# Kernel optimization log

Hardware: AMD Instinct MI355X
Metric: run time of the kernel (lower is better)

The kernel has to match this reference:

```python
import jax, jax.numpy as jnp
import numpy as np

B, T, I, H = 64, 256, 512, 800
RATE = 0.5


def setup_inputs() -> dict:
    key = jax.random.key(0)
    ks = jax.random.split(key, 9)
    x = jax.random.normal(ks[0], (B, T, I), dtype=jnp.float32)
    # Keras LSTM dropout: 4 per-gate Bernoulli masks on the input, constant over time
    mask_f = jax.random.bernoulli(ks[1], 1.0 - RATE, (B, 4, I)).astype(jnp.float32) / (1.0 - RATE)
    mask_b = jax.random.bernoulli(ks[2], 1.0 - RATE, (B, 4, I)).astype(jnp.float32) / (1.0 - RATE)
    s_w = 1.0 / np.sqrt(I)
    s_u = 1.0 / np.sqrt(H)
    W_f = jax.random.normal(ks[3], (I, 4 * H), dtype=jnp.float32) * s_w
    U_f = jax.random.normal(ks[4], (H, 4 * H), dtype=jnp.float32) * s_u
    W_b = jax.random.normal(ks[5], (I, 4 * H), dtype=jnp.float32) * s_w
    U_b = jax.random.normal(ks[6], (H, 4 * H), dtype=jnp.float32) * s_u
    # Keras unit_forget_bias: forget-gate bias = 1 (gate order i, f, c, o)
    b = jnp.concatenate([jnp.zeros(H), jnp.ones(H), jnp.zeros(H), jnp.zeros(H)]).astype(jnp.float32)
    return {"x": x, "mask_f": mask_f, "mask_b": mask_b,
            "W_f": W_f, "U_f": U_f, "b_f": b, "W_b": W_b, "U_b": U_b, "b_b": b}


def _lstm(x, W, U, b, mask):
    """x:(B,T,I) W:(I,4H) U:(H,4H) b:(4H,) mask:(B,4,I) -> (B,T,H), h, c."""
    b_, t_, i_ = x.shape
    h_ = U.shape[0]
    # per-gate input dropout, projections precomputed for all timesteps
    xd = x[:, :, None, :] * mask[:, None, :, :]                 # (B,T,4,I)
    proj = jnp.einsum('btgi,igh->btgh', xd, W.reshape(i_, 4, h_))
    proj = proj + b.reshape(4, h_)                              # (B,T,4,H)

    def step(carry, p):
        h, c = carry
        z = p + (h @ U).reshape(b_, 4, h_)                      # (B,4,H)
        i = jax.nn.sigmoid(z[:, 0])
        f = jax.nn.sigmoid(z[:, 1])
        g = jnp.tanh(z[:, 2])
        o = jax.nn.sigmoid(z[:, 3])
        c = f * c + i * g
        h = o * jnp.tanh(c)
        return (h, c), h

    h0 = jnp.zeros((b_, h_), x.dtype)
    c0 = jnp.zeros((b_, h_), x.dtype)
    (h, c), Hs = jax.lax.scan(step, (h0, c0), jnp.swapaxes(proj, 0, 1))
    return jnp.swapaxes(Hs, 0, 1), h, c


def reference(x, mask_f, mask_b, W_f, U_f, b_f, W_b, U_b, b_b):
    H1, h1, c1 = _lstm(x, W_f, U_f, b_f, mask_f)
    # go_backwards=True: process reversed sequence; Keras returns outputs in
    # processing (reversed) order and the model concatenates directly.
    H2, h2, c2 = _lstm(x[:, ::-1], W_b, U_b, b_b, mask_b)
    Hcat = jnp.concatenate([H1, H2], axis=2)
    hcat = jnp.concatenate([h1, h2], axis=1)
    ccat = jnp.concatenate([c1, c2], axis=1)
    return (Hcat, hcat, ccat)
```

## Files before the change

### kernel.cpp

```cpp
#include <hip/hip_runtime.h>


#define TDIM 256
#define IDIM 512
#define HDIM 800
#define H4   3200

typedef __bf16 bf16;
typedef __bf16 bf16x8 __attribute__((ext_vector_type(8)));
typedef __bf16 bf16x4 __attribute__((ext_vector_type(4)));
typedef float  f32x4  __attribute__((ext_vector_type(4)));
typedef unsigned int u32x4 __attribute__((ext_vector_type(4)));
typedef unsigned int u32x2 __attribute__((ext_vector_type(2)));

#define OFF_UPK   0ull
#define OFF_WPK   10240000ull
#define OFF_PROJB 16793600ull
#define OFF_HA    121651200ull
#define OFF_FLAGS 174284800ull
#define WS_NEED   174297600ull

__device__ __forceinline__ float sigf(float x)   { return 1.0f / (1.0f + __expf(-x)); }
__device__ __forceinline__ float tanhf_f(float x){ return 2.0f / (1.0f + __expf(-2.0f*x)) - 1.0f; }

__device__ __forceinline__ void store_b128_sc1(void* p, u32x4 v) {
    asm volatile("global_store_dwordx4 %0, %1, off sc1" :: "v"(p), "v"(v) : "memory");
}

__global__ __launch_bounds__(256) void kinit(uint4* __restrict__ ha0,
                                             uint4* __restrict__ flg) {
    int idx = blockIdx.x * 256 + threadIdx.x;
    if (idx < 12800) ha0[idx] = uint4{0u, 0u, 0u, 0u};
    else if (idx < 13600) flg[idx - 12800] = uint4{0u, 0u, 0u, 0u};
}

__global__ __launch_bounds__(64) void kpack(const float* __restrict__ Sf,
                                            const float* __restrict__ Sb,
                                            bf16* __restrict__ dst, int nkt) {
    int bx = blockIdx.x;
    int kt = bx % nkt; int rest = bx / nkt;
    int nt = rest % 200; int d = rest / 200;
    const float* S = d ? Sb : Sf;
    int l  = threadIdx.x;
    int n  = nt * 16 + (l & 15);
    int k0 = kt * 32 + (l >> 4) * 8;
    bf16x8 v;
#pragma unroll
    for (int j = 0; j < 8; ++j) v[j] = (bf16)S[(size_t)(k0 + j) * H4 + n];
    *(bf16x8*)(dst + ((size_t)bx * 64 + l) * 8) = v;
}

#define K1ROW 520
__global__ __launch_bounds__(256, 1) void kproj(
    const float* __restrict__ x, const float* __restrict__ mf, const float* __restrict__ mb,
    const bf16* __restrict__ wpk, const float* __restrict__ biasf, const float* __restrict__ biasb,
    bf16* __restrict__ projf, bf16* __restrict__ projb) {
    __shared__ bf16 sA[64 * K1ROW];

    int bx = blockIdx.x;
    int jj = bx % 5; int tt = (bx / 5) & 3; int g = (bx / 20) & 3;
    int b  = (bx / 80) & 63; int d = bx / 5120;

    int t  = threadIdx.x;
    int wv = t >> 6, l = t & 63;

    const float* mask = (d ? mb : mf) + (size_t)(b * 4 + g) * IDIM;
    int k = l * 8;
    float4 m0 = *(const float4*)(mask + k);
    float4 m1 = *(const float4*)(mask + k + 4);

    for (int it = 0; it < 16; ++it) {
        int trow = it * 4 + wv;
        int tg   = tt * 64 + trow;
        int te   = d ? (255 - tg) : tg;
        const float* xs = x + ((size_t)b * TDIM + te) * IDIM + k;
        float4 x0 = *(const float4*)xs;
        float4 x1 = *(const float4*)(xs + 4);
        bf16x8 v;
        v[0] = (bf16)(x0.x * m0.x); v[1] = (bf16)(x0.y * m0.y);
        v[2] = (bf16)(x0.z * m0.z); v[3] = (bf16)(x0.w * m0.w);
        v[4] = (bf16)(x1.x * m1.x); v[5] = (bf16)(x1.y * m1.y);
        v[6] = (bf16)(x1.z * m1.z); v[7] = (bf16)(x1.w * m1.w);
        *(bf16x8*)(&sA[trow * K1ROW + k]) = v;
    }
    __syncthreads();

    f32x4 acc[10];
#pragma unroll
    for (int nt = 0; nt < 10; ++nt) acc[nt] = f32x4{0.f, 0.f, 0.f, 0.f};

    int NTbase = g * 50 + jj * 10;
    const bf16* wb = wpk + ((size_t)d * 200 + NTbase) * 16 * 512 + l * 8;
    for (int kt = 0; kt < 16; ++kt) {
        bf16x8 a = *(const bf16x8*)(&sA[(wv * 16 + (l & 15)) * K1ROW + kt * 32 + (l >> 4) * 8]);
#pragma unroll
        for (int nt = 0; nt < 10; ++nt) {
            bf16x8 bw = *(const bf16x8*)(wb + ((size_t)nt * 16 + kt) * 512);
            acc[nt] = __builtin_amdgcn_mfma_f32_16x16x32_bf16(a, bw, acc[nt], 0, 0, 0);
        }
    }

    const float* bias = d ? biasb : biasf;
    bf16* dst = d ? projb : projf;
    int row0 = tt * 64 + wv * 16 + ((l >> 4) * 4);
#pragma unroll
    for (int nt = 0; nt < 10; ++nt) {
        int jr = jj * 160 + nt * 16 + (l & 15);
        float bv = bias[g * HDIM + jr];
#pragma unroll
        for (int r = 0; r < 4; ++r) {
            int trow = row0 + r;
            dst[((size_t)b * TDIM + trow) * H4 + (size_t)jr * 4 + g] = (bf16)(acc[nt][r] + bv);
        }
    }
}

__global__ __launch_bounds__(256, 1) void krecur(
    const bf16* __restrict__ upk,
    const bf16* __restrict__ projf, const bf16* __restrict__ projb,
    bf16* __restrict__ hA, int* __restrict__ flags,
    float* __restrict__ out) {
    extern __shared__ char ldsraw[];
    bf16* uLds = (bf16*)ldsraw;
    __shared__ bf16 sh2[4][16][24];

    int bx = blockIdx.x;
    int jt = bx % 50; int d = bx / 50;
    int tid = threadIdx.x;
    int w  = tid >> 6;
    int l  = tid & 63;
    int lm = l & 15, q = l >> 4;
    int j0 = jt * 16;
    int jcol = j0 + lm;
    int kt0 = jt >> 1, qbase = (jt & 1) * 2;

    bf16x8 ureg[50];
#pragma unroll
    for (int g = 0; g < 2; ++g)
#pragma unroll
        for (int kt = 0; kt < 25; ++kt) {
            bf16x8 v = *(const bf16x8*)(
                upk + (((size_t)(d * 200 + g * 50 + jt)) * 25 + kt) * 512 + (size_t)l * 8);
            u32x4 u = __builtin_bit_cast(u32x4, v);
            asm volatile("" : "+v"(u));
            ureg[g * 25 + kt] = __builtin_bit_cast(bf16x8, u);
        }

    if (w < 2) {
        const bf16* ug = upk + (((size_t)(d * 200 + (w + 2) * 50 + jt)) * 25) * 512 + (size_t)l * 8;
        bf16* udst = uLds + (size_t)w * 25 * 512 + (size_t)l * 8;
#pragma unroll
        for (int kt = 0; kt < 25; ++kt) {
            bf16x8 v = *(const bf16x8*)(ug + (size_t)kt * 512);
            *(bf16x8*)(udst + (size_t)kt * 512) = v;
        }
    }
    __syncthreads();

    const char* prbase = (const char*)(d ? projb : projf);

    int f1, f2;
    if (d == 0) { f1 = (l < 50) ? l : 49; f2 = f1; }
    else        { f1 = l; f2 = (l < 36) ? (64 + l) : l; }
    int fi1 = (f1 * 4 + w) * 8;
    int fi2 = (f2 * 4 + w) * 8;
    int myflag = (bx * 4 + w) * 8;

    float hprev[4], cst[4];
#pragma unroll
    for (int r = 0; r < 4; ++r) { hprev[r] = 0.f; cst[r] = 0.f; }

    size_t prOff = (size_t)j0 * 8 + (size_t)lm * 8;

#pragma unroll 1
    for (int s = 0; s < 256; ++s) {
        u32x2 pr[4];
#pragma unroll
        for (int r = 0; r < 4; ++r) {
            int b = w * 16 + q * 4 + r;
            pr[r] = __builtin_nontemporal_load(
                (const u32x2*)(prbase + ((size_t)b * TDIM + s) * 6400 + prOff));
        }

        if (s > 0) {
            for (;;) {
                int a  = __hip_atomic_load(flags + fi1, __ATOMIC_RELAXED, __HIP_MEMORY_SCOPE_AGENT);
                int b2 = __hip_atomic_load(flags + fi2, __ATOMIC_RELAXED, __HIP_MEMORY_SCOPE_AGENT);
                if (__all((a >= s) && (b2 >= s))) break;
                __builtin_amdgcn_s_sleep(2);
            }
        }
        asm volatile("" ::: "memory");

        const bf16* hin = hA + (size_t)s * 102400 + (size_t)d * 51200
                             + (size_t)w * 512 + (size_t)l * 8;
        bf16x8 af[25];
#pragma unroll
        for (int kt = 0; kt < 25; ++kt)
            af[kt] = *(const bf16x8*)(hin + (size_t)kt * 2048);

        if (s > 0) {
#pragma unroll
            for (int r = 0; r < 4; ++r) {
                int b = w * 16 + q * 4 + r;
                __builtin_nontemporal_store(hprev[r],
                    &out[((size_t)b * TDIM + (s - 1)) * 1600 + d * HDIM + jcol]);
            }
        }

        f32x4 acc[4];
#pragma unroll
        for (int g = 0; g < 4; ++g) acc[g] = f32x4{0.f, 0.f, 0.f, 0.f};

        const bf16* ul = uLds + (size_t)l * 8;
#pragma unroll
        for (int kt = 0; kt < 25; ++kt) {
            acc[0] = __builtin_amdgcn_mfma_f32_16x16x32_bf16(af[kt], ureg[kt],      acc[0], 0, 0, 0);
            acc[1] = __builtin_amdgcn_mfma_f32_16x16x32_bf16(af[kt], ureg[25 + kt], acc[1], 0, 0, 0);
            bf16x8 b2 = *(const bf16x8*)(ul + (size_t)kt * 512);
            bf16x8 b3 = *(const bf16x8*)(ul + (size_t)(25 + kt) * 512);
            acc[2] = __builtin_amdgcn_mfma_f32_16x16x32_bf16(af[kt], b2, acc[2], 0, 0, 0);
            acc[3] = __builtin_amdgcn_mfma_f32_16x16x32_bf16(af[kt], b3, acc[3], 0, 0, 0);
        }

#pragma unroll
        for (int r = 0; r < 4; ++r) {
            bf16x4 p4 = __builtin_bit_cast(bf16x4, pr[r]);
            float zi = acc[0][r] + (float)p4[0];
            float zf = acc[1][r] + (float)p4[1];
            float zg = acc[2][r] + (float)p4[2];
            float zo = acc[3][r] + (float)p4[3];
            float ig = sigf(zi), fg = sigf(zf), gg = tanhf_f(zg), og = sigf(zo);
            float cn = fg * cst[r] + ig * gg;
            cst[r] = cn;
            float h = og * tanhf_f(cn);
            hprev[r] = h;
            sh2[w][q * 4 + r][lm] = (bf16)h;
        }

        if (l < 32) {
            int qq = l >> 4;
            bf16x8 hv = *(const bf16x8*)(&sh2[w][lm][qq * 8]);
            int qp = qbase + qq;
            bf16* hAout = hA + (size_t)(s + 1) * 102400 + (size_t)d * 51200
                             + (size_t)(kt0 * 4 + w) * 512;
            store_b128_sc1(hAout + (size_t)(qp * 16 + lm) * 8, __builtin_bit_cast(u32x4, hv));
        }
        asm volatile("s_waitcnt vmcnt(0)" ::: "memory");
        if (l == 0)
            __hip_atomic_store(flags + myflag, s + 1, __ATOMIC_RELAXED, __HIP_MEMORY_SCOPE_AGENT);
    }

    for (;;) {
        int a  = __hip_atomic_load(flags + fi1, __ATOMIC_RELAXED, __HIP_MEMORY_SCOPE_AGENT);
        int b2 = __hip_atomic_load(flags + fi2, __ATOMIC_RELAXED, __HIP_MEMORY_SCOPE_AGENT);
        if (__all((a >= 256) && (b2 >= 256))) break;
        __builtin_amdgcn_s_sleep(2);
    }
    asm volatile("" ::: "memory");

#pragma unroll
    for (int r = 0; r < 4; ++r) {
        int b = w * 16 + q * 4 + r;
        out[((size_t)b * TDIM + 255) * 1600 + d * HDIM + jcol] = hprev[r];
        out[26214400u + (size_t)b * 1600 + d * HDIM + jcol] = hprev[r];
        out[26316800u + (size_t)b * 1600 + d * HDIM + jcol] = cst[r];
    }
}

extern "C" void kernel_launch(void* const* d_in, const int* in_sizes, int n_in,
                              void* d_out, int out_size, void* d_ws, size_t ws_size,
                              hipStream_t stream) {
    const float* x   = (const float*)d_in[0];
    const float* mf  = (const float*)d_in[1];
    const float* mb  = (const float*)d_in[2];
    const float* Wf  = (const float*)d_in[3];
    const float* Uf  = (const float*)d_in[4];
    const float* bf_ = (const float*)d_in[5];
    const float* Wb  = (const float*)d_in[6];
    const float* Ub  = (const float*)d_in[7];
    const float* bb_ = (const float*)d_in[8];

    if (ws_size < (size_t)WS_NEED) return;

    char*  ws    = (char*)d_ws;
    bf16*  upk   = (bf16*)(ws + OFF_UPK);
    bf16*  wpk   = (bf16*)(ws + OFF_WPK);
    bf16*  projb = (bf16*)(ws + OFF_PROJB);
    bf16*  hA    = (bf16*)(ws + OFF_HA);
    int*   flags = (int*)(ws + OFF_FLAGS);
    float* out   = (float*)d_out;
    bf16*  projf = (bf16*)d_out;

    static bool attr_set = false;
    if (!attr_set) {
        (void)hipFuncSetAttribute((const void*)krecur,
                                  hipFuncAttributeMaxDynamicSharedMemorySize, 51200);
        attr_set = true;
    }

    kinit<<<54, 256, 0, stream>>>((uint4*)(ws + OFF_HA), (uint4*)(ws + OFF_FLAGS));
    kpack<<<10000, 64, 0, stream>>>(Uf, Ub, upk, 25);
    kpack<<<6400, 64, 0, stream>>>(Wf, Wb, wpk, 16);
    kproj<<<10240, 256, 0, stream>>>(x, mf, mb, wpk, bf_, bb_, projf, projb);
    krecur<<<100, 256, 51200, stream>>>(upk, projf, projb, hA, flags, out);
}
```

Measured before the change: 2.227 ms.

## Decouple direction flag waits and defer output stores past the signal

Each wave now polls only its own direction's 50 producer flags on the critical path, and stops reloading lanes whose flags are already satisfied. The backward direction waits on forward-direction flags only after it has published its own step, just before its output store, which keeps the two scans ordered for output writes without stalling the recurrence. The output store of the previous h moves after the flag publish, and the poll sleep is shortened. The aim is to cut per-step latency on the serial recurrence, at the cost of more polling traffic and a more fragile ordering argument.

```diff
diff --git a/kernel.cpp b/kernel.cpp
--- a/kernel.cpp
+++ b/kernel.cpp
@@ -159,12 +159,12 @@
 
     const char* prbase = (const char*)(d ? projb : projf);
 
-    int f1, f2;
-    if (d == 0) { f1 = (l < 50) ? l : 49; f2 = f1; }
-    else        { f1 = l; f2 = (l < 36) ? (64 + l) : l; }
-    int fi1 = (f1 * 4 + w) * 8;
-    int fi2 = (f2 * 4 + w) * 8;
+    int lc = (l < 50) ? l : 49;
+    int fiOwn = ((d * 50 + lc) * 4 + w) * 8;
+    int fiFwd = (lc * 4 + w) * 8;
     int myflag = (bx * 4 + w) * 8;
+    int lastA = 0;
+    int lastF = 0;
 
     float hprev[4], cst[4];
 #pragma unroll
@@ -183,12 +183,14 @@
         }
 
         if (s > 0) {
-            for (;;) {
-                int a  = __hip_atomic_load(flags + fi1, __ATOMIC_RELAXED, __HIP_MEMORY_SCOPE_AGENT);
-                int b2 = __hip_atomic_load(flags + fi2, __ATOMIC_RELAXED, __HIP_MEMORY_SCOPE_AGENT);
-                if (__all((a >= s) && (b2 >= s))) break;
-                __builtin_amdgcn_s_sleep(2);
+            int a = lastA;
+            while (!__all(a >= s)) {
+                if (a < s)
+                    a = __hip_atomic_load(flags + fiOwn, __ATOMIC_RELAXED, __HIP_MEMORY_SCOPE_AGENT);
+                if (__all(a >= s)) break;
+                __builtin_amdgcn_s_sleep(1);
             }
+            lastA = a;
         }
         asm volatile("" ::: "memory");
 
@@ -198,15 +200,6 @@
 #pragma unroll
         for (int kt = 0; kt < 25; ++kt)
             af[kt] = *(const bf16x8*)(hin + (size_t)kt * 2048);
-
-        if (s > 0) {
-#pragma unroll
-            for (int r = 0; r < 4; ++r) {
-                int b = w * 16 + q * 4 + r;
-                __builtin_nontemporal_store(hprev[r],
-                    &out[((size_t)b * TDIM + (s - 1)) * 1600 + d * HDIM + jcol]);
-            }
-        }
 
         f32x4 acc[4];
 #pragma unroll
@@ -223,6 +216,9 @@
             acc[3] = __builtin_amdgcn_mfma_f32_16x16x32_bf16(af[kt], b3, acc[3], 0, 0, 0);
         }
 
+        float hout[4];
+#pragma unroll
+        for (int r = 0; r < 4; ++r) hout[r] = hprev[r];
 #pragma unroll
         for (int r = 0; r < 4; ++r) {
             bf16x4 p4 = __builtin_bit_cast(bf16x4, pr[r]);
@@ -249,15 +245,38 @@
         asm volatile("s_waitcnt vmcnt(0)" ::: "memory");
         if (l == 0)
             __hip_atomic_store(flags + myflag, s + 1, __ATOMIC_RELAXED, __HIP_MEMORY_SCOPE_AGENT);
-    }
-
-    for (;;) {
-        int a  = __hip_atomic_load(flags + fi1, __ATOMIC_RELAXED, __HIP_MEMORY_SCOPE_AGENT);
-        int b2 = __hip_atomic_load(flags + fi2, __ATOMIC_RELAXED, __HIP_MEMORY_SCOPE_AGENT);
-        if (__all((a >= 256) && (b2 >= 256))) break;
-        __builtin_amdgcn_s_sleep(2);
-    }
-    asm volatile("" ::: "memory");
+
+        if (s > 0) {
+            if (d == 1) {
+                int fA = lastF;
+                while (!__all(fA >= s)) {
+                    if (fA < s)
+                        fA = __hip_atomic_load(flags + fiFwd, __ATOMIC_RELAXED, __HIP_MEMORY_SCOPE_AGENT);
+                    if (__all(fA >= s)) break;
+                    __builtin_amdgcn_s_sleep(1);
+                }
+                lastF = fA;
+                asm volatile("" ::: "memory");
+            }
+#pragma unroll
+            for (int r = 0; r < 4; ++r) {
+                int b = w * 16 + q * 4 + r;
+                __builtin_nontemporal_store(hout[r],
+                    &out[((size_t)b * TDIM + (s - 1)) * 1600 + d * HDIM + jcol]);
+            }
+        }
+    }
+
+    {
+        int fA = (d == 0) ? lastA : lastF;
+        while (!__all(fA >= 256)) {
+            if (fA < 256)
+                fA = __hip_atomic_load(flags + fiFwd, __ATOMIC_RELAXED, __HIP_MEMORY_SCOPE_AGENT);
+            if (__all(fA >= 256)) break;
+            __builtin_amdgcn_s_sleep(1);
+        }
+        asm volatile("" ::: "memory");
+    }
 
 #pragma unroll
     for (int r = 0; r < 4; ++r) {
```

After: 2.938 ms. +32.0%, slower.
